# Kernel optimization log

Measured on AMD Instinct MI355X. Metric: run time of the kernel, lower is better.

Reference implementation:

```python
import jax, jax.numpy as jnp
import numpy as np

DIM, H, KV, HD = 2048, 32, 8, 64
NREP = H // KV
EPS = 1e-6
NEG = -1e30


def _rope(x, cos, sin):
    # x: [B,S,h,HD], cos/sin: [S,HD//2]
    xr, xi = x[..., 0::2], x[..., 1::2]
    c = cos[None, :, None, :]
    s = sin[None, :, None, :]
    out = jnp.stack([xr * c - xi * s, xr * s + xi * c], axis=-1)
    return out.reshape(x.shape)


def _rmsnorm(x, w):
    xf = x.astype(jnp.float32)
    inv = jax.lax.rsqrt(jnp.mean(xf * xf, axis=-1, keepdims=True) + EPS)
    return (xf * inv * w).astype(x.dtype)


def setup_inputs() -> dict:
    key = jax.random.key(0)
    ks = jax.random.split(key, 9)
    B, S = 1, 2048
    x = jax.random.normal(ks[0], (B, S, DIM), jnp.float32)
    cos = jax.random.uniform(ks[1], (S, HD // 2), jnp.float32)
    sin = jax.random.uniform(ks[2], (S, HD // 2), jnp.float32)
    sc = 1.0 / np.sqrt(DIM)
    wq = jax.random.normal(ks[3], (DIM, DIM), jnp.float32) * sc
    wk = jax.random.normal(ks[4], (KV * HD, DIM), jnp.float32) * sc
    wv = jax.random.normal(ks[5], (KV * HD, DIM), jnp.float32) * sc
    wo = jax.random.normal(ks[6], (DIM, DIM), jnp.float32) * sc
    wg = jax.random.normal(ks[7], (DIM, DIM), jnp.float32) * sc
    qn = jnp.ones((HD,), jnp.float32)
    kn = jnp.ones((HD,), jnp.float32)
    return {"x": x, "cos": cos, "sin": sin, "wq": wq, "wk": wk, "wv": wv,
            "wo": wo, "wg": wg, "qn": qn, "kn": kn}


def reference(x, cos, sin, wq, wk, wv, wo, wg, qn, kn):
    B, S, _ = x.shape
    q = (x @ wq.T).reshape(B, S, H, HD)
    k = (x @ wk.T).reshape(B, S, KV, HD)
    v = (x @ wv.T).reshape(B, S, KV, HD)
    q = _rope(q, cos, sin)
    k = _rope(k, cos, sin)
    q = _rmsnorm(q, qn)
    k = _rmsnorm(k, kn)
    # GQA without materializing repeat_kv: head h = g*NREP + r uses kv head g
    qg = q.reshape(B, S, KV, NREP, HD)
    scale = 1.0 / np.sqrt(HD)
    scores = jnp.einsum('bqgrd,bkgd->bgrqk', qg, k) * scale  # [B,KV,NREP,S,S]
    causal = jnp.tril(jnp.ones((S, S), bool))
    scores = jnp.where(causal, scores, NEG)
    attn = jax.nn.softmax(scores, axis=-1)
    o = jnp.einsum('bgrqk,bkgd->bqgrd', attn, v).reshape(B, S, DIM)
    o = o * jax.nn.sigmoid(x @ wg.T)
    return o @ wo.T
```

## Files before the change

kernel.cpp:

```cpp
#include <hip/hip_runtime.h>
#include <stdint.h>

typedef unsigned short u16;
typedef __bf16 bf16x8 __attribute__((ext_vector_type(8)));
typedef float f32x4 __attribute__((ext_vector_type(4)));

__device__ __forceinline__ float bf2f(u16 u) {
  union { unsigned int i; float f; } v; v.i = ((unsigned int)u) << 16; return v.f;
}
__device__ __forceinline__ u16 f2bf(float f) {
  union { float f; unsigned int i; } v; v.f = f;
  unsigned int r = v.i + 0x7fffu + ((v.i >> 16) & 1u);
  return (u16)(r >> 16);
}
__device__ __forceinline__ u16 f2bf_trunc(float f) {
  union { float f; unsigned int i; } v; v.f = f;
  return (u16)(v.i >> 16);
}
__device__ __forceinline__ void ld16(const void* g, void* l) {
  __builtin_amdgcn_global_load_lds(
      (const __attribute__((address_space(1))) unsigned int*)g,
      (__attribute__((address_space(3))) unsigned int*)l, 16, 0, 0);
}

__global__ __launch_bounds__(256) void k_cast(
    const float* __restrict__ s0, u16* __restrict__ d0,
    const float* __restrict__ s1, u16* __restrict__ d1,
    const float* __restrict__ s2, u16* __restrict__ d2,
    const float* __restrict__ s3, u16* __restrict__ d3,
    const float* __restrict__ s4, u16* __restrict__ d4,
    const float* __restrict__ s5, u16* __restrict__ d5)
{
  int b = blockIdx.x;
  const float* s; u16* d;
  if (b < 4096)       { s = s0; d = d0; }
  else if (b < 8192)  { s = s1; d = d1; b -= 4096; }
  else if (b < 9216)  { s = s2; d = d2; b -= 8192; }
  else if (b < 10240) { s = s3; d = d3; b -= 9216; }
  else if (b < 14336) { s = s4; d = d4; b -= 10240; }
  else                { s = s5; d = d5; b -= 14336; }
  const int i = (b * 256 + threadIdx.x) * 4;
  const float4 v = *(const float4*)(s + i);
  ushort4 o;
  o.x = f2bf(v.x); o.y = f2bf(v.y); o.z = f2bf(v.z); o.w = f2bf(v.w);
  *(ushort4*)(d + i) = o;
}

template <typename OT>
__device__ __forceinline__ void gemm_body(
    const u16* __restrict__ A, int lda,
    const u16* __restrict__ B, int ldb,
    OT* __restrict__ C, int ldc, int K,
    u16* As, u16* Bs)
{
  const int tid = threadIdx.x;
  const int wave = tid >> 6, lane = tid & 63;
  const int lrow = lane >> 2;
  const int lcol = (lane & 3) * 8;
  const int wrow = (wave >> 1) * 64, wcol = (wave & 1) * 64;
  const int fr = lane & 15, fq = (lane >> 4) * 8;

  f32x4 acc[4][4];
  const f32x4 z = {0.f, 0.f, 0.f, 0.f};
  for (int i = 0; i < 4; i++) for (int j = 0; j < 4; j++) acc[i][j] = z;

  const u16* Ag = A + (size_t)(wave * 32 + lrow) * lda + lcol;
  const u16* Bg = B + (size_t)(wave * 32 + lrow) * ldb + lcol;
  u16* Asw = As + wave * 1024;
  u16* Bsw = Bs + wave * 1024;

  for (int k0 = 0; k0 < K; k0 += 32) {
    ld16(Ag + k0, Asw);
    ld16(Ag + k0 + (size_t)16 * lda, Asw + 512);
    ld16(Bg + k0, Bsw);
    ld16(Bg + k0 + (size_t)16 * ldb, Bsw + 512);
    __syncthreads();
    bf16x8 af[4], bfr[4];
    for (int i = 0; i < 4; i++) af[i]  = *(const bf16x8*)&As[(wrow + i * 16 + fr) * 32 + fq];
    for (int i = 0; i < 4; i++) bfr[i] = *(const bf16x8*)&Bs[(wcol + i * 16 + fr) * 32 + fq];
    for (int mi = 0; mi < 4; mi++)
      for (int ni = 0; ni < 4; ni++)
        acc[mi][ni] = __builtin_amdgcn_mfma_f32_16x16x32_bf16(af[mi], bfr[ni], acc[mi][ni], 0, 0, 0);
    __syncthreads();
  }
  const int er = (lane >> 4) * 4, ec = lane & 15;
  for (int mi = 0; mi < 4; mi++)
    for (int ni = 0; ni < 4; ni++)
      for (int r = 0; r < 4; r++) {
        const float v = acc[mi][ni][r];
        OT* p = C + (size_t)(wrow + mi * 16 + er + r) * ldc + wcol + ni * 16 + ec;
        if constexpr (sizeof(OT) == 2) *p = (OT)f2bf(v); else *p = (OT)v;
      }
}

__global__ __launch_bounds__(256) void k_gemm_qkvg(
    const u16* __restrict__ x, const u16* __restrict__ wq, const u16* __restrict__ wk,
    const u16* __restrict__ wv, const u16* __restrict__ wg, u16* __restrict__ out)
{
  __shared__ __align__(16) u16 As[128 * 32];
  __shared__ __align__(16) u16 Bs[128 * 32];
  const int m0 = blockIdx.x * 128;
  const int c0 = blockIdx.y * 128;
  const u16* B; int br;
  if (c0 < 2048)      { B = wq; br = c0; }
  else if (c0 < 2560) { B = wk; br = c0 - 2048; }
  else if (c0 < 3072) { B = wv; br = c0 - 2560; }
  else                { B = wg; br = c0 - 3072; }
  gemm_body<u16>(x + (size_t)m0 * 2048, 2048, B + (size_t)br * 2048, 2048,
                 out + (size_t)m0 * 5120 + c0, 5120, 2048, As, Bs);
}

__global__ __launch_bounds__(256) void k_gemm_out(
    const u16* __restrict__ a, const u16* __restrict__ wo, float* __restrict__ out)
{
  __shared__ __align__(16) u16 As[128 * 32];
  __shared__ __align__(16) u16 Bs[128 * 32];
  const int m0 = blockIdx.x * 128;
  const int c0 = blockIdx.y * 128;
  gemm_body<float>(a + (size_t)m0 * 2048, 2048, wo + (size_t)c0 * 2048, 2048,
                   out + (size_t)m0 * 2048 + c0, 2048, 2048, As, Bs);
}

__global__ __launch_bounds__(256) void k_rope_norm(
    u16* __restrict__ qkvg, const float* __restrict__ cosp, const float* __restrict__ sinp,
    const float* __restrict__ qn, const float* __restrict__ kn)
{
  const int wid = (blockIdx.x * 256 + threadIdx.x) >> 6;
  const int lane = threadIdx.x & 63;
  const int s = wid / 20, hp = wid - s * 20;
  const int h = hp * 2 + (lane >> 5);
  const int j = lane & 31;
  u16* base; const float* wn;
  if (h < 32) { base = qkvg + (size_t)s * 5120 + h * 64;                wn = qn; }
  else        { base = qkvg + (size_t)s * 5120 + 2048 + (h - 32) * 64; wn = kn; }
  const unsigned int u = *(const unsigned int*)(base + 2 * j);
  const float xr = bf2f((u16)(u & 0xffffu)), xi = bf2f((u16)(u >> 16));
  const float c = cosp[s * 32 + j], sn = sinp[s * 32 + j];
  const float o0 = xr * c - xi * sn;
  const float o1 = xr * sn + xi * c;
  float ss = o0 * o0 + o1 * o1;
  for (int m = 1; m <= 16; m <<= 1) ss += __shfl_xor(ss, m, 64);
  const float inv = rsqrtf(ss * (1.0f / 64.0f) + 1e-6f);
  const u16 r0 = f2bf(o0 * inv * wn[2 * j]);
  const u16 r1 = f2bf(o1 * inv * wn[2 * j + 1]);
  *(unsigned int*)(base + 2 * j) = (unsigned int)r0 | ((unsigned int)r1 << 16);
}

__global__ __launch_bounds__(256) void k_vtrans(const u16* __restrict__ qkvg, u16* __restrict__ vt)
{
  __shared__ u16 Ls[64 * 72];
  const int s0 = blockIdx.x * 64, g0 = blockIdx.y * 64;
  const int tid = threadIdx.x;
  const int lr = tid >> 4, lc = (tid & 15) * 4;
  for (int p = 0; p < 4; p++) {
    const int r = p * 16 + lr;
    *(ushort4*)&Ls[r * 72 + lc] = *(const ushort4*)&qkvg[(size_t)(s0 + r) * 5120 + 2560 + g0 + lc];
  }
  __syncthreads();
  for (int p = 0; p < 4; p++) {
    const int r = p * 16 + lr;
    ushort4 o;
    o.x = Ls[(lc + 0) * 72 + r];
    o.y = Ls[(lc + 1) * 72 + r];
    o.z = Ls[(lc + 2) * 72 + r];
    o.w = Ls[(lc + 3) * 72 + r];
    *(ushort4*)&vt[(size_t)(g0 + r) * 2048 + s0 + lc] = o;
  }
}

__global__ __launch_bounds__(256) void k_attn_part(
    const u16* __restrict__ qkvg, const u16* __restrict__ vt,
    u16* __restrict__ part, float* __restrict__ ml)
{
  __shared__ __align__(16) u16 Ks[128 * 64];
  __shared__ __align__(16) u16 Vs[64 * 128];
  __shared__ __align__(16) u16 Ps[64 * 132];
  const int c = blockIdx.x, h = blockIdx.y, g = h >> 2;
  int qt, ci;
  if (c < 8)       { qt = c;                 ci = 0; }
  else if (c < 24) { qt = 8 + ((c - 8) >> 1);  ci = (c - 8) & 1; }
  else if (c < 48) { qt = 16 + (c - 24) / 3;   ci = (c - 24) % 3; }
  else             { qt = 24 + ((c - 48) >> 2); ci = (c - 48) & 3; }
  const int kb0 = ci * 512;
  const int kend = min(kb0 + 512, (qt + 1) * 64);
  const int q0 = qt * 64;
  const int tid = threadIdx.x, wave = tid >> 6, lane = tid & 63;
  const int fr = lane & 15, kg = lane >> 4, fq = kg * 8;
  const int sx = fr & 7;

  {
    const u16* Qg = qkvg + (size_t)(q0 + wave * 16 + (lane >> 3)) * 5120 + h * 64 + (lane & 7) * 8;
    ld16(Qg, Ks + wave * 1024);
    ld16(Qg + (size_t)8 * 5120, Ks + wave * 1024 + 512);
  }
  __syncthreads();
  const bf16x8 aq0 = *(const bf16x8*)&Ks[(wave * 16 + fr) * 64 + fq];
  const bf16x8 aq1 = *(const bf16x8*)&Ks[(wave * 16 + fr) * 64 + 32 + fq];
  __syncthreads();

  f32x4 o[4];
  const f32x4 z = {0.f, 0.f, 0.f, 0.f};
  for (int i = 0; i < 4; i++) o[i] = z;
  float lsum[4] = {0.f, 0.f, 0.f, 0.f};
  const int qrow = q0 + wave * 16 + kg * 4;

  const int krl = wave * 8 + (lane >> 3);
  const int kcg = (lane & 7) ^ (krl & 7);
  const int vrl = wave * 4 + kg;
  const int vcg = fr ^ (vrl & 7);

  for (int kb = kb0; kb < kend; kb += 128) {
    {
      const u16* Kg = qkvg + (size_t)(kb + krl) * 5120 + 2048 + g * 64 + kcg * 8;
      for (int i = 0; i < 4; i++)
        ld16(Kg + (size_t)(i * 32) * 5120, Ks + (i * 32 + wave * 8) * 64);
    }
    {
      const u16* Vg = vt + (size_t)(g * 64 + vrl) * 2048 + kb + vcg * 8;
      for (int i = 0; i < 4; i++)
        ld16(Vg + (size_t)(i * 16) * 2048, Vs + (i * 16 + wave * 4) * 128);
    }
    __syncthreads();

    f32x4 sc[8];
    for (int i = 0; i < 8; i++) sc[i] = z;
    for (int ni = 0; ni < 8; ni++) {
      const bf16x8 bk0 = *(const bf16x8*)&Ks[(ni * 16 + fr) * 64 + (kg ^ sx) * 8];
      const bf16x8 bk1 = *(const bf16x8*)&Ks[(ni * 16 + fr) * 64 + ((kg + 4) ^ sx) * 8];
      sc[ni] = __builtin_amdgcn_mfma_f32_16x16x32_bf16(aq0, bk0, sc[ni], 0, 0, 0);
      sc[ni] = __builtin_amdgcn_mfma_f32_16x16x32_bf16(aq1, bk1, sc[ni], 0, 0, 0);
    }

    for (int r = 0; r < 4; r++) {
      float ls = 0.f;
      for (int ni = 0; ni < 8; ni++) {
        const int key = kb + ni * 16 + fr;
        float p = __expf(fmaf(sc[ni][r], 0.125f, -8.0f));
        p = (key <= qrow + r) ? p : 0.f;
        ls += p;
        Ps[(wave * 16 + kg * 4 + r) * 132 + ni * 16 + fr] = f2bf_trunc(p);
      }
      lsum[r] += ls;
    }

    for (int k0 = 0; k0 < 128; k0 += 32) {
      const bf16x8 ap = *(const bf16x8*)&Ps[(wave * 16 + fr) * 132 + k0 + fq];
      for (int ni = 0; ni < 4; ni++) {
        const bf16x8 bv = *(const bf16x8*)&Vs[(ni * 16 + fr) * 128 + (((k0 >> 3) + kg) ^ sx) * 8];
        o[ni] = __builtin_amdgcn_mfma_f32_16x16x32_bf16(ap, bv, o[ni], 0, 0, 0);
      }
    }
    __syncthreads();
  }

  const int pbase = (h * 80 + c) * 4096;
  for (int r = 0; r < 4; r++) {
    float L = lsum[r];
    for (int m = 1; m <= 8; m <<= 1) L += __shfl_xor(L, m, 64);
    const int rl = wave * 16 + kg * 4 + r;
    for (int ni = 0; ni < 4; ni++)
      part[pbase + rl * 64 + ni * 16 + fr] = f2bf(o[ni][r]);
    if (fr == 0) ml[(h * 80 + c) * 64 + rl] = L;
  }
}

__global__ __launch_bounds__(256) void k_attn_comb(
    const u16* __restrict__ part, const float* __restrict__ ml,
    const u16* __restrict__ qkvg, u16* __restrict__ aout)
{
  const int qt = blockIdx.x, h = blockIdx.y;
  const int w = threadIdx.x >> 6, lane = threadIdx.x & 63;
  int cb, nch;
  if (qt < 8)       { cb = qt;               nch = 1; }
  else if (qt < 16) { cb = 8 + 2 * (qt - 8);  nch = 2; }
  else if (qt < 24) { cb = 24 + 3 * (qt - 16); nch = 3; }
  else              { cb = 48 + 4 * (qt - 24); nch = 4; }
  for (int r = 0; r < 16; r++) {
    const int rl = w * 16 + r;
    const int row = qt * 64 + rl;
    float L = 0.f, o = 0.f;
    for (int cc = 0; cc < nch; cc++) {
      L += ml[(h * 80 + cb + cc) * 64 + rl];
      o += bf2f(part[(h * 80 + cb + cc) * 4096 + rl * 64 + lane]);
    }
    const float gv = bf2f(qkvg[(size_t)row * 5120 + 3072 + h * 64 + lane]);
    const float sig = 1.0f / (1.0f + __expf(-gv));
    aout[(size_t)row * 2048 + h * 64 + lane] = f2bf(o / L * sig);
  }
}

extern "C" void kernel_launch(void* const* d_in, const int* in_sizes, int n_in,
                              void* d_out, int out_size, void* d_ws, size_t ws_size,
                              hipStream_t stream)
{
  const float* x  = (const float*)d_in[0];
  const float* cs = (const float*)d_in[1];
  const float* sn = (const float*)d_in[2];
  const float* wq = (const float*)d_in[3];
  const float* wk = (const float*)d_in[4];
  const float* wv = (const float*)d_in[5];
  const float* wo = (const float*)d_in[6];
  const float* wg = (const float*)d_in[7];
  const float* qn = (const float*)d_in[8];
  const float* kn = (const float*)d_in[9];
  float* out = (float*)d_out;

  u16* xb   = (u16*)d_ws;
  u16* wqb  = xb  + (size_t)4194304;
  u16* wkb  = wqb + (size_t)4194304;
  u16* wvb  = wkb + (size_t)1048576;
  u16* wgb  = wvb + (size_t)1048576;
  u16* wob  = wgb + (size_t)4194304;
  u16* qkvg = wob + (size_t)4194304;
  u16* vt   = qkvg + (size_t)2048 * 5120;
  u16* aws  = vt   + (size_t)512 * 2048;

  u16*   part = xb;
  float* ml   = (float*)(xb + (size_t)32 * 80 * 4096);

  k_cast<<<dim3(18432), 256, 0, stream>>>(x, xb, wq, wqb, wk, wkb, wv, wvb, wo, wob, wg, wgb);
  k_gemm_qkvg<<<dim3(16, 40), 256, 0, stream>>>(xb, wqb, wkb, wvb, wgb, qkvg);
  k_rope_norm<<<dim3(2048 * 20 / 4), 256, 0, stream>>>(qkvg, cs, sn, qn, kn);
  k_vtrans<<<dim3(32, 8), 256, 0, stream>>>(qkvg, vt);
  k_attn_part<<<dim3(80, 32), 256, 0, stream>>>(qkvg, vt, part, ml);
  k_attn_comb<<<dim3(32, 32), 256, 0, stream>>>(part, ml, qkvg, aws);
  k_gemm_out<<<dim3(16, 16), 256, 0, stream>>>(aws, wob, out);
}
```

Before: 309.4 us.

## Double GEMM K-step to 64 with XOR-swizzled LDS layout; merge rope and V-transpose

The shared GEMM body now loads a 64-wide K slice per iteration, which halves the number of barrier pairs. It stores tiles in LDS using an XOR swizzle on 16-byte column groups so the MFMA fragment reads avoid bank conflicts. LDS per block doubles to 32 KB, which may reduce occupancy. The rope/rmsnorm kernel and the V-transpose kernel are also merged into one launch by splitting on block index, saving one kernel launch.

```diff
diff --git a/kernel.cpp b/kernel.cpp
--- a/kernel.cpp
+++ b/kernel.cpp
@@ -55,35 +55,40 @@
 {
   const int tid = threadIdx.x;
   const int wave = tid >> 6, lane = tid & 63;
-  const int lrow = lane >> 2;
-  const int lcol = (lane & 3) * 8;
   const int wrow = (wave >> 1) * 64, wcol = (wave & 1) * 64;
-  const int fr = lane & 15, fq = (lane >> 4) * 8;
+  const int fr = lane & 15, kg = lane >> 4;
+  const int srl = lane >> 3;
+  const int scg = (lane & 7) ^ srl;
 
   f32x4 acc[4][4];
   const f32x4 z = {0.f, 0.f, 0.f, 0.f};
   for (int i = 0; i < 4; i++) for (int j = 0; j < 4; j++) acc[i][j] = z;
 
-  const u16* Ag = A + (size_t)(wave * 32 + lrow) * lda + lcol;
-  const u16* Bg = B + (size_t)(wave * 32 + lrow) * ldb + lcol;
-  u16* Asw = As + wave * 1024;
-  u16* Bsw = Bs + wave * 1024;
-
-  for (int k0 = 0; k0 < K; k0 += 32) {
-    ld16(Ag + k0, Asw);
-    ld16(Ag + k0 + (size_t)16 * lda, Asw + 512);
-    ld16(Bg + k0, Bsw);
-    ld16(Bg + k0 + (size_t)16 * ldb, Bsw + 512);
-    __syncthreads();
-    bf16x8 af[4], bfr[4];
-    for (int i = 0; i < 4; i++) af[i]  = *(const bf16x8*)&As[(wrow + i * 16 + fr) * 32 + fq];
-    for (int i = 0; i < 4; i++) bfr[i] = *(const bf16x8*)&Bs[(wcol + i * 16 + fr) * 32 + fq];
-    for (int mi = 0; mi < 4; mi++)
-      for (int ni = 0; ni < 4; ni++)
-        acc[mi][ni] = __builtin_amdgcn_mfma_f32_16x16x32_bf16(af[mi], bfr[ni], acc[mi][ni], 0, 0, 0);
-    __syncthreads();
-  }
-  const int er = (lane >> 4) * 4, ec = lane & 15;
+  const u16* Ag = A + (size_t)(wave * 8 + srl) * lda + scg * 8;
+  const u16* Bg = B + (size_t)(wave * 8 + srl) * ldb + scg * 8;
+  u16* Asw = As + wave * 8 * 64;
+  u16* Bsw = Bs + wave * 8 * 64;
+  const int sxr = fr & 7;
+
+  for (int k0 = 0; k0 < K; k0 += 64) {
+    for (int i = 0; i < 4; i++) {
+      ld16(Ag + k0 + (size_t)(i * 32) * lda, Asw + i * 32 * 64);
+      ld16(Bg + k0 + (size_t)(i * 32) * ldb, Bsw + i * 32 * 64);
+    }
+    __syncthreads();
+    bf16x8 af[4][2], bfr[4][2];
+    for (int i = 0; i < 4; i++)
+      for (int h = 0; h < 2; h++) {
+        af[i][h]  = *(const bf16x8*)&As[(wrow + i * 16 + fr) * 64 + (((h * 4 + kg) ^ sxr)) * 8];
+        bfr[i][h] = *(const bf16x8*)&Bs[(wcol + i * 16 + fr) * 64 + (((h * 4 + kg) ^ sxr)) * 8];
+      }
+    for (int h = 0; h < 2; h++)
+      for (int mi = 0; mi < 4; mi++)
+        for (int ni = 0; ni < 4; ni++)
+          acc[mi][ni] = __builtin_amdgcn_mfma_f32_16x16x32_bf16(af[mi][h], bfr[ni][h], acc[mi][ni], 0, 0, 0);
+    __syncthreads();
+  }
+  const int er = kg * 4, ec = fr;
   for (int mi = 0; mi < 4; mi++)
     for (int ni = 0; ni < 4; ni++)
       for (int r = 0; r < 4; r++) {
@@ -97,8 +102,8 @@
     const u16* __restrict__ x, const u16* __restrict__ wq, const u16* __restrict__ wk,
     const u16* __restrict__ wv, const u16* __restrict__ wg, u16* __restrict__ out)
 {
-  __shared__ __align__(16) u16 As[128 * 32];
-  __shared__ __align__(16) u16 Bs[128 * 32];
+  __shared__ __align__(16) u16 As[128 * 64];
+  __shared__ __align__(16) u16 Bs[128 * 64];
   const int m0 = blockIdx.x * 128;
   const int c0 = blockIdx.y * 128;
   const u16* B; int br;
@@ -113,58 +118,58 @@
 __global__ __launch_bounds__(256) void k_gemm_out(
     const u16* __restrict__ a, const u16* __restrict__ wo, float* __restrict__ out)
 {
-  __shared__ __align__(16) u16 As[128 * 32];
-  __shared__ __align__(16) u16 Bs[128 * 32];
+  __shared__ __align__(16) u16 As[128 * 64];
+  __shared__ __align__(16) u16 Bs[128 * 64];
   const int m0 = blockIdx.x * 128;
   const int c0 = blockIdx.y * 128;
   gemm_body<float>(a + (size_t)m0 * 2048, 2048, wo + (size_t)c0 * 2048, 2048,
                    out + (size_t)m0 * 2048 + c0, 2048, 2048, As, Bs);
 }
 
-__global__ __launch_bounds__(256) void k_rope_norm(
+__global__ __launch_bounds__(256) void k_prep(
     u16* __restrict__ qkvg, const float* __restrict__ cosp, const float* __restrict__ sinp,
-    const float* __restrict__ qn, const float* __restrict__ kn)
-{
-  const int wid = (blockIdx.x * 256 + threadIdx.x) >> 6;
-  const int lane = threadIdx.x & 63;
-  const int s = wid / 20, hp = wid - s * 20;
-  const int h = hp * 2 + (lane >> 5);
-  const int j = lane & 31;
-  u16* base; const float* wn;
-  if (h < 32) { base = qkvg + (size_t)s * 5120 + h * 64;                wn = qn; }
-  else        { base = qkvg + (size_t)s * 5120 + 2048 + (h - 32) * 64; wn = kn; }
-  const unsigned int u = *(const unsigned int*)(base + 2 * j);
-  const float xr = bf2f((u16)(u & 0xffffu)), xi = bf2f((u16)(u >> 16));
-  const float c = cosp[s * 32 + j], sn = sinp[s * 32 + j];
-  const float o0 = xr * c - xi * sn;
-  const float o1 = xr * sn + xi * c;
-  float ss = o0 * o0 + o1 * o1;
-  for (int m = 1; m <= 16; m <<= 1) ss += __shfl_xor(ss, m, 64);
-  const float inv = rsqrtf(ss * (1.0f / 64.0f) + 1e-6f);
-  const u16 r0 = f2bf(o0 * inv * wn[2 * j]);
-  const u16 r1 = f2bf(o1 * inv * wn[2 * j + 1]);
-  *(unsigned int*)(base + 2 * j) = (unsigned int)r0 | ((unsigned int)r1 << 16);
-}
-
-__global__ __launch_bounds__(256) void k_vtrans(const u16* __restrict__ qkvg, u16* __restrict__ vt)
+    const float* __restrict__ qn, const float* __restrict__ kn, u16* __restrict__ vt)
 {
   __shared__ u16 Ls[64 * 72];
-  const int s0 = blockIdx.x * 64, g0 = blockIdx.y * 64;
-  const int tid = threadIdx.x;
-  const int lr = tid >> 4, lc = (tid & 15) * 4;
-  for (int p = 0; p < 4; p++) {
-    const int r = p * 16 + lr;
-    *(ushort4*)&Ls[r * 72 + lc] = *(const ushort4*)&qkvg[(size_t)(s0 + r) * 5120 + 2560 + g0 + lc];
-  }
-  __syncthreads();
-  for (int p = 0; p < 4; p++) {
-    const int r = p * 16 + lr;
-    ushort4 o;
-    o.x = Ls[(lc + 0) * 72 + r];
-    o.y = Ls[(lc + 1) * 72 + r];
-    o.z = Ls[(lc + 2) * 72 + r];
-    o.w = Ls[(lc + 3) * 72 + r];
-    *(ushort4*)&vt[(size_t)(g0 + r) * 2048 + s0 + lc] = o;
+  if (blockIdx.x < 10240) {
+    const int wid = (blockIdx.x * 256 + threadIdx.x) >> 6;
+    const int lane = threadIdx.x & 63;
+    const int s = wid / 20, hp = wid - s * 20;
+    const int h = hp * 2 + (lane >> 5);
+    const int j = lane & 31;
+    u16* base; const float* wn;
+    if (h < 32) { base = qkvg + (size_t)s * 5120 + h * 64;                wn = qn; }
+    else        { base = qkvg + (size_t)s * 5120 + 2048 + (h - 32) * 64; wn = kn; }
+    const unsigned int u = *(const unsigned int*)(base + 2 * j);
+    const float xr = bf2f((u16)(u & 0xffffu)), xi = bf2f((u16)(u >> 16));
+    const float c = cosp[s * 32 + j], sn = sinp[s * 32 + j];
+    const float o0 = xr * c - xi * sn;
+    const float o1 = xr * sn + xi * c;
+    float ss = o0 * o0 + o1 * o1;
+    for (int m = 1; m <= 16; m <<= 1) ss += __shfl_xor(ss, m, 64);
+    const float inv = rsqrtf(ss * (1.0f / 64.0f) + 1e-6f);
+    const u16 r0 = f2bf(o0 * inv * wn[2 * j]);
+    const u16 r1 = f2bf(o1 * inv * wn[2 * j + 1]);
+    *(unsigned int*)(base + 2 * j) = (unsigned int)r0 | ((unsigned int)r1 << 16);
+  } else {
+    const int bb = blockIdx.x - 10240;
+    const int s0 = (bb & 31) * 64, g0 = (bb >> 5) * 64;
+    const int tid = threadIdx.x;
+    const int lr = tid >> 4, lc = (tid & 15) * 4;
+    for (int p = 0; p < 4; p++) {
+      const int r = p * 16 + lr;
+      *(ushort4*)&Ls[r * 72 + lc] = *(const ushort4*)&qkvg[(size_t)(s0 + r) * 5120 + 2560 + g0 + lc];
+    }
+    __syncthreads();
+    for (int p = 0; p < 4; p++) {
+      const int r = p * 16 + lr;
+      ushort4 o;
+      o.x = Ls[(lc + 0) * 72 + r];
+      o.y = Ls[(lc + 1) * 72 + r];
+      o.z = Ls[(lc + 2) * 72 + r];
+      o.w = Ls[(lc + 3) * 72 + r];
+      *(ushort4*)&vt[(size_t)(g0 + r) * 2048 + s0 + lc] = o;
+    }
   }
 }
 
@@ -320,8 +325,7 @@
 
   k_cast<<<dim3(18432), 256, 0, stream>>>(x, xb, wq, wqb, wk, wkb, wv, wvb, wo, wob, wg, wgb);
   k_gemm_qkvg<<<dim3(16, 40), 256, 0, stream>>>(xb, wqb, wkb, wvb, wgb, qkvg);
-  k_rope_norm<<<dim3(2048 * 20 / 4), 256, 0, stream>>>(qkvg, cs, sn, qn, kn);
-  k_vtrans<<<dim3(32, 8), 256, 0, stream>>>(qkvg, vt);
+  k_prep<<<dim3(10240 + 256), 256, 0, stream>>>(qkvg, cs, sn, qn, kn, vt);
   k_attn_part<<<dim3(80, 32), 256, 0, stream>>>(qkvg, vt, part, ml);
   k_attn_comb<<<dim3(32, 32), 256, 0, stream>>>(part, ml, qkvg, aws);
   k_gemm_out<<<dim3(16, 16), 256, 0, stream>>>(aws, wob, out);
```

Result: faster. 295.4 us (-4.5%).
